# Performance work log

Measured on AMD Instinct MI355X. Metric: run time of the kernel, lower is better.

## Reference

```python
import jax, jax.numpy as jnp
import numpy as np

H = 256      # hidden_size
B = 32       # batch
T = 4096     # timesteps / graph nodes
E = 8192     # edges per graph
PATH = 1
EXPAND_WEIGHT = 0.1
MODE = 'son'


def setup_inputs() -> dict:
    key = jax.random.key(0)
    ks = jax.random.split(key, 6)
    hidden = jax.random.normal(ks[0], (B, H), jnp.float32)
    encoder_outputs = jax.random.normal(ks[1], (T, B, H), jnp.float32)
    edges_src = jax.random.randint(ks[2], (B, E), 0, T)
    edges_dst = jax.random.randint(ks[3], (B, E), 0, T)
    # nn.Linear(2H, 2H) params (kaiming-uniform-ish scale) and the v vector
    lim = 1.0 / np.sqrt(2 * H)
    W_attn = jax.random.uniform(ks[4], (2 * H, 2 * H), jnp.float32, -lim, lim)
    b_attn = jnp.zeros((2 * H,), jnp.float32)
    v = jax.random.uniform(ks[5], (2 * H,), jnp.float32, -lim, lim)
    return {"hidden": hidden, "encoder_outputs": encoder_outputs,
            "edges_src": edges_src, "edges_dst": edges_dst,
            "W_attn": W_attn, "b_attn": b_attn, "v": v}


def reference(hidden, encoder_outputs, edges_src, edges_dst, W_attn, b_attn, v):
    Bb, Hh = hidden.shape
    Tt = encoder_outputs.shape[0]
    # h: [B, T, H] (hidden repeated over timesteps); enc: [B, T, H]
    h = jnp.broadcast_to(hidden[:, None, :], (Bb, Tt, Hh))
    enc = jnp.transpose(encoder_outputs, (1, 0, 2))
    # score: tanh(Linear(cat)) then v . energy -> [B, T]
    energy = jnp.tanh(jnp.concatenate([h, enc], axis=2) @ W_attn.T + b_attn)
    scores = jnp.einsum('btd,d->bt', energy, v)
    w = jax.nn.softmax(scores, axis=1)
    # expand_attn: scatter-add along graph edges, skipping consecutive (y == x+1)
    mask = (edges_dst != edges_src + 1).astype(w.dtype)  # [B, E]
    def scatter(wb, src, dst, m):
        if MODE == 'son':
            return jnp.zeros_like(wb).at[dst].add(wb[src] * m)
        else:
            return jnp.zeros_like(wb).at[src].add(wb[dst] * m)
    for _ in range(PATH):
        w = jax.vmap(scatter)(w, edges_src, edges_dst, mask) * EXPAND_WEIGHT
    return w[:, None, :]  # [B, 1, T]
```

## Files before the change

kernel.cpp:

```cpp
#include <hip/hip_runtime.h>
#include <hip/hip_bf16.h>

typedef __attribute__((ext_vector_type(8))) short bf16x8;
typedef __attribute__((ext_vector_type(4))) float f32x4;

#define HD 256
#define NB 32
#define NT 4096
#define NE 8192
#define N2 512

static __device__ __forceinline__ unsigned short f2bf(float f) {
  unsigned int u = __float_as_uint(f);
  u += 0x7fff + ((u >> 16) & 1);
  return (unsigned short)(u >> 16);
}
static __device__ __forceinline__ short4 cvt4(float4 a) {
  return make_short4((short)f2bf(a.x), (short)f2bf(a.y),
                     (short)f2bf(a.z), (short)f2bf(a.w));
}
static __device__ __forceinline__ float fast_tanh(float x) {
  float e = __builtin_amdgcn_exp2f(x * 2.8853900817779268f);
  return __builtin_fmaf(-2.f, __builtin_amdgcn_rcpf(e + 1.f), 1.f);
}
static __device__ __forceinline__ bf16x8 pack8(float4 a, float4 b) {
  union { bf16x8 v; unsigned int u[4]; } r;
  r.u[0] = (__float_as_uint(a.y) & 0xffff0000u) | (__float_as_uint(a.x) >> 16);
  r.u[1] = (__float_as_uint(a.w) & 0xffff0000u) | (__float_as_uint(a.z) >> 16);
  r.u[2] = (__float_as_uint(b.y) & 0xffff0000u) | (__float_as_uint(b.x) >> 16);
  r.u[3] = (__float_as_uint(b.w) & 0xffff0000u) | (__float_as_uint(b.z) >> 16);
  return r.v;
}

#define GLDS16(g, l)                                                       \
  __builtin_amdgcn_global_load_lds(                                        \
      (const __attribute__((address_space(1))) unsigned int*)(g),          \
      (__attribute__((address_space(3))) unsigned int*)(l), 16, 0, 0)

__global__ __launch_bounds__(256) void prep(
    const float* __restrict__ hidden, const float* __restrict__ Wattn,
    const float* __restrict__ battn, float* __restrict__ cvecT,
    short* __restrict__ Wbf) {
  const int tid = threadIdx.x;
  if (blockIdx.x < 256) {
    __shared__ float Ws[64 * 260];
    __shared__ float Hs[HD];
    const int chunk = blockIdx.x & 7;
    const int b = blockIdx.x >> 3;
#pragma unroll
    for (int it = 0; it < 16; ++it) {
      int f = it * 1024 + tid * 4;
      int i = f >> 8, k = f & 255;
      float4 w4 = *(const float4*)(Wattn + (chunk * 64 + i) * N2 + k);
      *(float4*)&Ws[i * 260 + k] = w4;
    }
    if (tid < 64)
      *(float4*)&Hs[tid * 4] = *(const float4*)(hidden + b * HD + tid * 4);
    __syncthreads();
    const int nl = tid >> 2;
    const int kb = (tid & 3) * 64;
    float sum = 0.f;
#pragma unroll
    for (int z = 0; z < 64; z += 4) {
      float4 h4 = *(const float4*)&Hs[kb + z];
      float4 w4 = *(const float4*)&Ws[nl * 260 + kb + z];
      sum = fmaf(h4.x, w4.x, sum);
      sum = fmaf(h4.y, w4.y, sum);
      sum = fmaf(h4.z, w4.z, sum);
      sum = fmaf(h4.w, w4.w, sum);
    }
    sum += __shfl_xor(sum, 1, 64);
    sum += __shfl_xor(sum, 2, 64);
    if ((tid & 3) == 0)
      cvecT[(chunk * 64 + nl) * NB + b] = sum + battn[chunk * 64 + nl];
  } else {
    int f = (blockIdx.x - 256) * 1024 + tid * 4;
    int n = f >> 8, k = f & 255;
    float4 w4 = *(const float4*)(Wattn + n * N2 + HD + k);
    *(short4*)(Wbf + f) = cvt4(w4);
  }
}

__global__ __launch_bounds__(256, 2) void score_gemm(
    const float* __restrict__ enc, const short* __restrict__ Wbf,
    const float* __restrict__ cvecT, const float* __restrict__ vvec,
    float* __restrict__ scores) {
  __shared__ float As[512 * 4];
  __shared__ short Bs[2048 * 8];
  __shared__ float part[4][64];
  const int tid = threadIdx.x;
  const int w = tid >> 6, lane = tid & 63, q = lane >> 4, m = lane & 15;
  const int row0 = blockIdx.x * 64;

  f32x4 acc[4][8];
#pragma unroll
  for (int mi = 0; mi < 4; ++mi)
#pragma unroll
    for (int nf = 0; nf < 8; ++nf) acc[mi][nf] = (f32x4){0.f, 0.f, 0.f, 0.f};

#pragma unroll 1
  for (int ks = 0; ks < 8; ++ks) {
    const int k0 = ks * 32;
    __syncthreads();
#pragma unroll
    for (int i = 0; i < 2; ++i) {
      const int S = (i * 4 + w) * 64 + lane;
      const int r = S >> 3;
      const int kc = (S & 7) ^ (r & 7);
      GLDS16(enc + (row0 + r) * HD + k0 + kc * 4, &As[(S & ~63) * 4]);
    }
#pragma unroll
    for (int i = 0; i < 8; ++i) {
      const int S = (i * 4 + w) * 64 + lane;
      const int n = S >> 2;
      const int kc = (S & 3) ^ ((n >> 1) & 3);
      GLDS16(Wbf + n * HD + k0 + kc * 8, &Bs[(S & ~63) * 8]);
    }
    __syncthreads();

    bf16x8 bfr[8];
#pragma unroll
    for (int nf = 0; nf < 8; ++nf) {
      const int n = w * 128 + nf * 16 + m;
      bfr[nf] = *(const bf16x8*)&Bs[(n * 4 + (q ^ ((n >> 1) & 3))) * 8];
    }
#pragma unroll
    for (int mi = 0; mi < 4; ++mi) {
      const int r = mi * 16 + m;
      float4 a0 = *(const float4*)&As[(r * 8 + ((2 * q) ^ (r & 7))) * 4];
      float4 a1 = *(const float4*)&As[(r * 8 + ((2 * q + 1) ^ (r & 7))) * 4];
      bf16x8 af = pack8(a0, a1);
#pragma unroll
      for (int nf = 0; nf < 8; ++nf)
        acc[mi][nf] = __builtin_amdgcn_mfma_f32_16x16x32_bf16(af, bfr[nf], acc[mi][nf], 0, 0, 0);
    }
  }

  float p[4][4];
#pragma unroll
  for (int mi = 0; mi < 4; ++mi)
#pragma unroll
    for (int j = 0; j < 4; ++j) p[mi][j] = 0.f;

#pragma unroll
  for (int nf = 0; nf < 8; ++nf) {
    const int n = w * 128 + nf * 16 + m;
    const float vv = vvec[n];
    const f32x4 cvA = *(const f32x4*)(cvecT + n * NB + 4 * q);
    const f32x4 cvB = *(const f32x4*)(cvecT + n * NB + 16 + 4 * q);
#pragma unroll
    for (int mi = 0; mi < 4; ++mi) {
      const f32x4 cv = (mi & 1) ? cvB : cvA;
#pragma unroll
      for (int j = 0; j < 4; ++j)
        p[mi][j] += fast_tanh(acc[mi][nf][j] + cv[j]) * vv;
    }
  }
#pragma unroll
  for (int mi = 0; mi < 4; ++mi) {
#pragma unroll
    for (int j = 0; j < 4; ++j) {
      float e = p[mi][j];
      e += __shfl_xor(e, 1, 64);
      e += __shfl_xor(e, 2, 64);
      e += __shfl_xor(e, 4, 64);
      e += __shfl_xor(e, 8, 64);
      if (m == 0) part[w][mi * 16 + 4 * q + j] = e;
    }
  }
  __syncthreads();
  if (tid < 64) {
    const int r = row0 + tid;
    scores[(r & 31) * NT + (r >> 5)] =
        part[0][tid] + part[1][tid] + part[2][tid] + part[3][tid];
  }
}

__global__ __launch_bounds__(1024) void softmax_norm(
    const float* __restrict__ sc, float* __restrict__ smax,
    float* __restrict__ sinv, float* __restrict__ out) {
  __shared__ float rtmp[16];
  __shared__ float rres;
  const int b = blockIdx.x;
  const int tid = threadIdx.x;
  const int wid = tid >> 6, lane = tid & 63;
  float s[4];
  float mx = -1e30f;
#pragma unroll
  for (int p = 0; p < 4; ++p) {
    s[p] = sc[b * NT + tid + p * 1024];
    mx = fmaxf(mx, s[p]);
  }
#pragma unroll
  for (int d = 32; d >= 1; d >>= 1) mx = fmaxf(mx, __shfl_xor(mx, d, 64));
  if (lane == 0) rtmp[wid] = mx;
  __syncthreads();
  if (tid == 0) {
    float mm = rtmp[0];
#pragma unroll
    for (int i = 1; i < 16; ++i) mm = fmaxf(mm, rtmp[i]);
    rres = mm;
  }
  __syncthreads();
  mx = rres;
  float sm = 0.f;
#pragma unroll
  for (int p = 0; p < 4; ++p) sm += __expf(s[p] - mx);
#pragma unroll
  for (int d = 32; d >= 1; d >>= 1) sm += __shfl_xor(sm, d, 64);
  if (lane == 0) rtmp[wid] = sm;
  __syncthreads();
  if (tid == 0) {
    float tt = 0.f;
#pragma unroll
    for (int i = 0; i < 16; ++i) tt += rtmp[i];
    smax[b] = mx;
    sinv[b] = 0.1f / tt;
  }
#pragma unroll
  for (int p = 0; p < 4; ++p) out[b * NT + tid + p * 1024] = 0.f;
}

__global__ __launch_bounds__(256) void scatter(
    const float* __restrict__ sc, const float* __restrict__ smax,
    const float* __restrict__ sinv, const int* __restrict__ esrc,
    const int* __restrict__ edst, float* __restrict__ out) {
  const int idx = blockIdx.x * 256 + threadIdx.x;
  const int b = idx >> 13, e = idx & (NE - 1);
  const int ss = esrc[b * NE + e];
  const int dd = edst[b * NE + e];
  const float wv = __expf(sc[b * NT + ss] - smax[b]) * sinv[b];
  if (dd != ss + 1) atomicAdd(out + b * NT + dd, wv);
}

extern "C" void kernel_launch(void* const* d_in, const int* in_sizes, int n_in,
                              void* d_out, int out_size, void* d_ws, size_t ws_size,
                              hipStream_t stream) {
  const float* hidden = (const float*)d_in[0];
  const float* enc    = (const float*)d_in[1];
  const int*   esrc   = (const int*)d_in[2];
  const int*   edst   = (const int*)d_in[3];
  const float* Wattn  = (const float*)d_in[4];
  const float* battn  = (const float*)d_in[5];
  const float* vvec   = (const float*)d_in[6];
  float* out = (float*)d_out;

  char* ws = (char*)d_ws;
  float* cvecT  = (float*)ws;
  short* Wbf    = (short*)(ws + 65536);
  float* scores = (float*)(ws + 65536 + 262144);
  float* smax   = (float*)(ws + 65536 + 262144 + 524288);
  float* sinv   = (float*)(ws + 65536 + 262144 + 524288 + 128);

  prep<<<384, 256, 0, stream>>>(hidden, Wattn, battn, cvecT, Wbf);
  score_gemm<<<(NB * NT) / 64, 256, 0, stream>>>(enc, Wbf, cvecT, vvec, scores);
  softmax_norm<<<NB, 1024, 0, stream>>>(scores, smax, sinv, out);
  scatter<<<(NB * NE) / 256, 256, 0, stream>>>(scores, smax, sinv, esrc, edst, out);
}
```

Measured before the change: 282.2 us.

## Preload full A tile once, stream B from global, fuse softmax with LDS scatter

The score GEMM now loads each block's entire 64x256 fp32 encoder tile into LDS once, up front, and reads the bf16 weight fragments straight from global memory into registers with double buffering. This removes the per-k-step barriers and the LDS staging of B. Separately, the softmax and scatter kernels are merged into one kernel per batch that keeps the normalized weights and an accumulator in LDS, does the scatter with LDS atomics, and writes the output once. The trade-off is higher LDS use per block (64KB for A plus 32KB in the fused kernel), which may cut occupancy, and B reads that now depend on the cache.

```diff
diff --git a/kernel.cpp b/kernel.cpp
--- a/kernel.cpp
+++ b/kernel.cpp
@@ -81,59 +81,65 @@
   }
 }
 
+static __device__ __forceinline__ void bload(bf16x8* dst, const short* __restrict__ Wbf,
+                                             int nbase, int q, int kk) {
+#pragma unroll
+  for (int nf = 0; nf < 8; ++nf)
+    dst[nf] = *(const bf16x8*)(Wbf + (nbase + nf * 16) * HD + kk * 32 + q * 8);
+}
+
+static __device__ __forceinline__ void kstep(f32x4 acc[4][8], const float4* As4,
+                                             const bf16x8* b, int m, int q, int ks) {
+#pragma unroll
+  for (int mi = 0; mi < 4; ++mi) {
+    const int r = mi * 16 + m;
+    const int cb = r * 64 + ks * 8;
+    float4 a0 = As4[cb + ((2 * q) ^ (r & 7))];
+    float4 a1 = As4[cb + ((2 * q + 1) ^ (r & 7))];
+    bf16x8 af = pack8(a0, a1);
+#pragma unroll
+    for (int nf = 0; nf < 8; ++nf)
+      acc[mi][nf] =
+          __builtin_amdgcn_mfma_f32_16x16x32_bf16(af, b[nf], acc[mi][nf], 0, 0, 0);
+  }
+}
+
 __global__ __launch_bounds__(256, 2) void score_gemm(
     const float* __restrict__ enc, const short* __restrict__ Wbf,
     const float* __restrict__ cvecT, const float* __restrict__ vvec,
     float* __restrict__ scores) {
-  __shared__ float As[512 * 4];
-  __shared__ short Bs[2048 * 8];
+  __shared__ float4 As4[64 * 64];
   __shared__ float part[4][64];
   const int tid = threadIdx.x;
   const int w = tid >> 6, lane = tid & 63, q = lane >> 4, m = lane & 15;
   const int row0 = blockIdx.x * 64;
 
+#pragma unroll
+  for (int i = 0; i < 16; ++i) {
+    const int r = i * 4 + w;
+    const int gc = (lane & ~7) | ((lane & 7) ^ (r & 7));
+    GLDS16(enc + (row0 + r) * HD + gc * 4, &As4[r * 64]);
+  }
+
   f32x4 acc[4][8];
 #pragma unroll
   for (int mi = 0; mi < 4; ++mi)
 #pragma unroll
     for (int nf = 0; nf < 8; ++nf) acc[mi][nf] = (f32x4){0.f, 0.f, 0.f, 0.f};
 
+  const int nbase = w * 128 + m;
+  bf16x8 b0[8], b1[8];
+  bload(b0, Wbf, nbase, q, 0);
+
+  __syncthreads();
+
 #pragma unroll 1
-  for (int ks = 0; ks < 8; ++ks) {
-    const int k0 = ks * 32;
-    __syncthreads();
-#pragma unroll
-    for (int i = 0; i < 2; ++i) {
-      const int S = (i * 4 + w) * 64 + lane;
-      const int r = S >> 3;
-      const int kc = (S & 7) ^ (r & 7);
-      GLDS16(enc + (row0 + r) * HD + k0 + kc * 4, &As[(S & ~63) * 4]);
-    }
-#pragma unroll
-    for (int i = 0; i < 8; ++i) {
-      const int S = (i * 4 + w) * 64 + lane;
-      const int n = S >> 2;
-      const int kc = (S & 3) ^ ((n >> 1) & 3);
-      GLDS16(Wbf + n * HD + k0 + kc * 8, &Bs[(S & ~63) * 8]);
-    }
-    __syncthreads();
-
-    bf16x8 bfr[8];
-#pragma unroll
-    for (int nf = 0; nf < 8; ++nf) {
-      const int n = w * 128 + nf * 16 + m;
-      bfr[nf] = *(const bf16x8*)&Bs[(n * 4 + (q ^ ((n >> 1) & 3))) * 8];
-    }
-#pragma unroll
-    for (int mi = 0; mi < 4; ++mi) {
-      const int r = mi * 16 + m;
-      float4 a0 = *(const float4*)&As[(r * 8 + ((2 * q) ^ (r & 7))) * 4];
-      float4 a1 = *(const float4*)&As[(r * 8 + ((2 * q + 1) ^ (r & 7))) * 4];
-      bf16x8 af = pack8(a0, a1);
-#pragma unroll
-      for (int nf = 0; nf < 8; ++nf)
-        acc[mi][nf] = __builtin_amdgcn_mfma_f32_16x16x32_bf16(af, bfr[nf], acc[mi][nf], 0, 0, 0);
-    }
+  for (int ks2 = 0; ks2 < 4; ++ks2) {
+    const int ks = ks2 * 2;
+    bload(b1, Wbf, nbase, q, ks + 1);
+    kstep(acc, As4, b0, m, q, ks);
+    if (ks2 < 3) bload(b0, Wbf, nbase, q, ks + 2);
+    kstep(acc, As4, b1, m, q, ks + 1);
   }
 
   float p[4][4];
@@ -176,14 +182,17 @@
   }
 }
 
-__global__ __launch_bounds__(1024) void softmax_norm(
-    const float* __restrict__ sc, float* __restrict__ smax,
-    float* __restrict__ sinv, float* __restrict__ out) {
+__global__ __launch_bounds__(1024) void softmax_scatter(
+    const float* __restrict__ sc, const int* __restrict__ esrc,
+    const int* __restrict__ edst, float* __restrict__ out) {
+  __shared__ float wls[NT];
+  __shared__ float accs[NT];
   __shared__ float rtmp[16];
-  __shared__ float rres;
+  __shared__ float rmax, rinv;
   const int b = blockIdx.x;
   const int tid = threadIdx.x;
   const int wid = tid >> 6, lane = tid & 63;
+
   float s[4];
   float mx = -1e30f;
 #pragma unroll
@@ -199,13 +208,17 @@
     float mm = rtmp[0];
 #pragma unroll
     for (int i = 1; i < 16; ++i) mm = fmaxf(mm, rtmp[i]);
-    rres = mm;
-  }
-  __syncthreads();
-  mx = rres;
+    rmax = mm;
+  }
+  __syncthreads();
+  mx = rmax;
+  float e[4];
   float sm = 0.f;
 #pragma unroll
-  for (int p = 0; p < 4; ++p) sm += __expf(s[p] - mx);
+  for (int p = 0; p < 4; ++p) {
+    e[p] = __expf(s[p] - mx);
+    sm += e[p];
+  }
 #pragma unroll
   for (int d = 32; d >= 1; d >>= 1) sm += __shfl_xor(sm, d, 64);
   if (lane == 0) rtmp[wid] = sm;
@@ -214,23 +227,28 @@
     float tt = 0.f;
 #pragma unroll
     for (int i = 0; i < 16; ++i) tt += rtmp[i];
-    smax[b] = mx;
-    sinv[b] = 0.1f / tt;
-  }
-#pragma unroll
-  for (int p = 0; p < 4; ++p) out[b * NT + tid + p * 1024] = 0.f;
-}
-
-__global__ __launch_bounds__(256) void scatter(
-    const float* __restrict__ sc, const float* __restrict__ smax,
-    const float* __restrict__ sinv, const int* __restrict__ esrc,
-    const int* __restrict__ edst, float* __restrict__ out) {
-  const int idx = blockIdx.x * 256 + threadIdx.x;
-  const int b = idx >> 13, e = idx & (NE - 1);
-  const int ss = esrc[b * NE + e];
-  const int dd = edst[b * NE + e];
-  const float wv = __expf(sc[b * NT + ss] - smax[b]) * sinv[b];
-  if (dd != ss + 1) atomicAdd(out + b * NT + dd, wv);
+    rinv = 0.1f / tt;
+  }
+  __syncthreads();
+  const float inv = rinv;
+#pragma unroll
+  for (int p = 0; p < 4; ++p) {
+    wls[tid + p * 1024] = e[p] * inv;
+    accs[tid + p * 1024] = 0.f;
+  }
+  __syncthreads();
+#pragma unroll
+  for (int i = 0; i < 8; ++i) {
+    const int eid = b * NE + tid + i * 1024;
+    const int ss = esrc[eid];
+    const int dd = edst[eid];
+    const float wv = wls[ss];
+    if (dd != ss + 1) atomicAdd(&accs[dd], wv);
+  }
+  __syncthreads();
+#pragma unroll
+  for (int p = 0; p < 4; ++p)
+    out[b * NT + tid + p * 1024] = accs[tid + p * 1024];
 }
 
 extern "C" void kernel_launch(void* const* d_in, const int* in_sizes, int n_in,
@@ -249,11 +267,8 @@
   float* cvecT  = (float*)ws;
   short* Wbf    = (short*)(ws + 65536);
   float* scores = (float*)(ws + 65536 + 262144);
-  float* smax   = (float*)(ws + 65536 + 262144 + 524288);
-  float* sinv   = (float*)(ws + 65536 + 262144 + 524288 + 128);
 
   prep<<<384, 256, 0, stream>>>(hidden, Wattn, battn, cvecT, Wbf);
   score_gemm<<<(NB * NT) / 64, 256, 0, stream>>>(enc, Wbf, cvecT, vvec, scores);
-  softmax_norm<<<NB, 1024, 0, stream>>>(scores, smax, sinv, out);
-  scatter<<<(NB * NE) / 256, 256, 0, stream>>>(scores, smax, sinv, esrc, edst, out);
-}
+  softmax_scatter<<<NB, 1024, 0, stream>>>(scores, esrc, edst, out);
+}
```

New measurement: 284.4 us. About the same (+0.8%).
